# Performance work log

Measured on AMD Instinct MI355X. Metric: run time of the kernel, lower is better.

## Reference

```python
import jax, jax.numpy as jnp
import numpy as np

KS = 15       # erosion kernel size (ones kernel -> flat erosion = local min)
R = 60        # guided filter box-blur size
EPS = 1e-4


def _box_blur(x, r):
    # kornia box_blur: same-size mean filter, reflect padding; even kernel pads
    # (r-1)//2 before and r-1-(r-1)//2 after, per kornia _compute_padding.
    pb = (r - 1) // 2
    pa = r - 1 - pb
    xp = jnp.pad(x, ((0, 0), (0, 0), (pb, pa), (pb, pa)), mode='reflect')
    one = jnp.asarray(0.0, x.dtype)
    s = jax.lax.reduce_window(xp, one, jax.lax.add, (1, 1, r, 1), (1, 1, 1, 1), 'VALID')
    s = jax.lax.reduce_window(s, one, jax.lax.add, (1, 1, 1, r), (1, 1, 1, 1), 'VALID')
    return s / jnp.asarray(r * r, x.dtype)


def _erosion(x, k):
    # kornia flat erosion with ones kernel, geodesic border: local min over kxk
    p = k // 2
    init = jnp.asarray(jnp.inf, x.dtype)
    pad = [(0, 0), (0, 0), (p, p), (p, p)]
    e = jax.lax.reduce_window(x, init, jax.lax.min, (1, 1, k, 1), (1, 1, 1, 1), [(0, 0), (0, 0), (p, p), (0, 0)])
    e = jax.lax.reduce_window(e, init, jax.lax.min, (1, 1, 1, k), (1, 1, 1, 1), [(0, 0), (0, 0), (0, 0), (p, p)])
    return e


def setup_inputs() -> dict:
    key = jax.random.key(0)
    I = jax.random.uniform(key, (8, 3, 1080, 1920), dtype=jnp.float32)
    return {"I": I}


def reference(I) -> jnp.ndarray:
    # dark channel: per-pixel min over the 3 channels  [B,1,H,W]
    dark = jnp.min(I, axis=1, keepdims=True)
    # guided_filter_plus(dark)
    d_im = _erosion(dark, KS)
    mean_I = _box_blur(d_im, R)
    mean_p = _box_blur(dark, R)
    mean_Ip = _box_blur(d_im * dark, R)
    cov_Ip = mean_Ip - mean_I * mean_p
    mean_II = _box_blur(d_im * d_im, R)
    var_I = mean_II - mean_I * mean_I
    a = cov_Ip / (var_I + EPS)
    b = mean_p - a * mean_I
    mean_a = _box_blur(a, R)
    mean_b = _box_blur(b, R)
    q = mean_a * d_im + mean_b
    return q
```

## Files before the change

kernel.cpp:

```cpp
#include <hip/hip_runtime.h>
#include <hip/hip_fp16.h>

#define HH 1080
#define WW 1920
#define NB 8
#define HWP (HH*WW)
#define NPX (NB*HWP)
#define NCX (WW/2)

__device__ __forceinline__ int reflH(int y){ int r = y < 0 ? -y : y; return r >= HH ? 2*HH-2-r : r; }
__device__ __forceinline__ int reflW(int x){ int r = x < 0 ? -x : x; return r >= WW ? 2*WW-2-r : r; }

__global__ __launch_bounds__(256) void k_dark(const float* __restrict__ I, __half* __restrict__ dark){
    int q = blockIdx.x*blockDim.x + threadIdx.x;
    if (q >= NPX/4) return;
    int base = q*4;
    int b = base / HWP;
    int p = base - b*HWP;
    const float* src = I + (size_t)b*3*HWP + p;
    float4 c0 = *(const float4*)(src);
    float4 c1 = *(const float4*)(src + HWP);
    float4 c2 = *(const float4*)(src + 2*HWP);
    float m0 = fminf(fminf(c0.x, c1.x), c2.x);
    float m1 = fminf(fminf(c0.y, c1.y), c2.y);
    float m2 = fminf(fminf(c0.z, c1.z), c2.z);
    float m3 = fminf(fminf(c0.w, c1.w), c2.w);
    __half2* dst = (__half2*)(dark + base);
    dst[0] = __floats2half2_rn(m0, m1);
    dst[1] = __floats2half2_rn(m2, m3);
}

#define EV_T 60
__global__ __launch_bounds__(256) void k_erosv(const __half* __restrict__ in, __half* __restrict__ out){
    int t = blockIdx.x*blockDim.x + threadIdx.x;
    if (t >= NCX*NB*(HH/EV_T)) return;
    int cx = t % NCX;
    int r  = t / NCX;
    int b  = r % NB;
    int y0 = (r / NB) * EV_T;
    const __half2* src = (const __half2*)(in  + (size_t)b*HWP) + cx;
    __half2*       dst = (__half2*)(out + (size_t)b*HWP) + cx;
    float2 w[15];
    #pragma unroll
    for (int k = 0; k < 14; ++k){
        int y = y0 - 7 + k;
        if (y >= 0 && y < HH) w[k] = __half22float2(src[(size_t)y*NCX]);
        else { w[k].x = 1e5f; w[k].y = 1e5f; }
    }
    for (int y = y0; y < y0 + EV_T; ++y){
        int yn = y + 7;
        if (yn < HH) w[14] = __half22float2(src[(size_t)yn*NCX]);
        else { w[14].x = 1e5f; w[14].y = 1e5f; }
        float ax[8], ay[8];
        #pragma unroll
        for (int k = 0; k < 7; ++k){ ax[k] = fminf(w[2*k].x, w[2*k+1].x); ay[k] = fminf(w[2*k].y, w[2*k+1].y); }
        ax[7] = w[14].x; ay[7] = w[14].y;
        #pragma unroll
        for (int k = 0; k < 4; ++k){ ax[k] = fminf(ax[k], ax[k+4]); ay[k] = fminf(ay[k], ay[k+4]); }
        float mx = fminf(fminf(ax[0], ax[1]), fminf(ax[2], ax[3]));
        float my = fminf(fminf(ay[0], ay[1]), fminf(ay[2], ay[3]));
        dst[(size_t)y*NCX] = __floats2half2_rn(mx, my);
        #pragma unroll
        for (int k = 0; k < 14; ++k) w[k] = w[k+1];
    }
}

__global__ __launch_bounds__(256) void k_erosh(const __half* __restrict__ in, __half* __restrict__ out){
    __shared__ __half2 lds[264];
    int bid = blockIdx.x;
    int seg = bid & 3;
    int y   = (bid >> 2) % HH;
    int b   = bid / (4*HH);
    int seg0 = seg * 512;
    const __half* row = in + (size_t)b*HWP + (size_t)y*WW;
    int tid = threadIdx.x;
    for (int slot = tid; slot < 264; slot += 256){
        int x = seg0 - 8 + 2*slot;
        __half2 v;
        if (x >= 0 && x + 1 < WW) v = *(const __half2*)(row + x);
        else {
            float lo = (x   >= 0 && x   < WW) ? __half2float(row[x])   : 1e5f;
            float hi = (x+1 >= 0 && x+1 < WW) ? __half2float(row[x+1]) : 1e5f;
            v = __floats2half2_rn(lo, hi);
        }
        lds[slot] = v;
    }
    __syncthreads();
    int x0 = seg0 + 2*tid;
    if (x0 >= WW) return;
    float v[18];
    #pragma unroll
    for (int k = 0; k < 9; ++k){
        float2 f = __half22float2(lds[tid + k]);
        v[2*k] = f.x; v[2*k+1] = f.y;
    }
    float c = v[2];
    #pragma unroll
    for (int k = 3; k <= 15; ++k) c = fminf(c, v[k]);
    float o0 = fminf(c, v[1]);
    float o1 = fminf(c, v[16]);
    *(__half2*)(out + (size_t)b*HWP + (size_t)y*WW + x0) = __floats2half2_rn(o0, o1);
}

#define BV_T 54
__global__ __launch_bounds__(256) void k_blurv4(const __half* __restrict__ pdim, const __half* __restrict__ pdark,
                                                __half* __restrict__ v0, __half* __restrict__ v1,
                                                __half* __restrict__ v2, __half* __restrict__ v3){
    int t = blockIdx.x*blockDim.x + threadIdx.x;
    if (t >= NCX*NB*(HH/BV_T)) return;
    int cx = t % NCX;
    int r  = t / NCX;
    int b  = r % NB;
    int y0 = (r / NB) * BV_T;
    size_t pb = (size_t)b*HWP;
    const __half2* pd = (const __half2*)(pdim  + pb) + cx;
    const __half2* pk = (const __half2*)(pdark + pb) + cx;
    __half2* o0 = (__half2*)(v0 + pb) + cx;
    __half2* o1 = (__half2*)(v1 + pb) + cx;
    __half2* o2 = (__half2*)(v2 + pb) + cx;
    __half2* o3 = (__half2*)(v3 + pb) + cx;

    float si0=0,si1=0,sp0=0,sp1=0,sip0=0,sip1=0,sii0=0,sii1=0;
    auto acc = [&](int yy, float sg){
        int yr = reflH(yy);
        float2 di = __half22float2(pd[(size_t)yr*NCX]);
        float2 dk = __half22float2(pk[(size_t)yr*NCX]);
        si0  += sg*di.x;        si1  += sg*di.y;
        sp0  += sg*dk.x;        sp1  += sg*dk.y;
        sip0 += sg*(di.x*dk.x); sip1 += sg*(di.y*dk.y);
        sii0 += sg*(di.x*di.x); sii1 += sg*(di.y*di.y);
    };
    const float inv = 1.0f/60.0f;
    for (int k = -29; k <= 30; ++k) acc(y0 + k, 1.0f);
    size_t off = (size_t)y0*NCX;
    o0[off] = __floats2half2_rn(si0*inv,  si1*inv);
    o1[off] = __floats2half2_rn(sp0*inv,  sp1*inv);
    o2[off] = __floats2half2_rn(sip0*inv, sip1*inv);
    o3[off] = __floats2half2_rn(sii0*inv, sii1*inv);
    for (int y = y0 + 1; y < y0 + BV_T; ++y){
        acc(y + 30, 1.0f);
        acc(y - 30, -1.0f);
        off = (size_t)y*NCX;
        o0[off] = __floats2half2_rn(si0*inv,  si1*inv);
        o1[off] = __floats2half2_rn(sp0*inv,  sp1*inv);
        o2[off] = __floats2half2_rn(sip0*inv, sip1*inv);
        o3[off] = __floats2half2_rn(sii0*inv, sii1*inv);
    }
}

__global__ __launch_bounds__(256) void k_blurv2(const __half* __restrict__ pa, const __half* __restrict__ pbf,
                                                __half* __restrict__ va, __half* __restrict__ vb){
    int t = blockIdx.x*blockDim.x + threadIdx.x;
    if (t >= NCX*NB*(HH/BV_T)) return;
    int cx = t % NCX;
    int r  = t / NCX;
    int b  = r % NB;
    int y0 = (r / NB) * BV_T;
    size_t pbase = (size_t)b*HWP;
    const __half2* p0 = (const __half2*)(pa  + pbase) + cx;
    const __half2* p1 = (const __half2*)(pbf + pbase) + cx;
    __half2* o0 = (__half2*)(va + pbase) + cx;
    __half2* o1 = (__half2*)(vb + pbase) + cx;
    float sa0=0,sa1=0,sb0=0,sb1=0;
    auto acc = [&](int yy, float sg){
        int yr = reflH(yy);
        float2 fa = __half22float2(p0[(size_t)yr*NCX]);
        float2 fb = __half22float2(p1[(size_t)yr*NCX]);
        sa0 += sg*fa.x; sa1 += sg*fa.y;
        sb0 += sg*fb.x; sb1 += sg*fb.y;
    };
    const float inv = 1.0f/60.0f;
    for (int k = -29; k <= 30; ++k) acc(y0 + k, 1.0f);
    size_t off = (size_t)y0*NCX;
    o0[off] = __floats2half2_rn(sa0*inv, sa1*inv);
    o1[off] = __floats2half2_rn(sb0*inv, sb1*inv);
    for (int y = y0 + 1; y < y0 + BV_T; ++y){
        acc(y + 30, 1.0f);
        acc(y - 30, -1.0f);
        off = (size_t)y*NCX;
        o0[off] = __floats2half2_rn(sa0*inv, sa1*inv);
        o1[off] = __floats2half2_rn(sb0*inv, sb1*inv);
    }
}

#define PADI(e) ((e) + ((e) >> 5))

__global__ __launch_bounds__(128) void k_blurh4(const __half* __restrict__ v0, const __half* __restrict__ v1,
                                                const __half* __restrict__ v2, const __half* __restrict__ v3,
                                                __half* __restrict__ pa, __half* __restrict__ pbf){
    __shared__ float lds[4][2048];
    int bid = blockIdx.x;
    int y = bid % HH;
    int b = bid / HH;
    size_t rb = (size_t)b*HWP + (size_t)y*WW;
    const __half* p0 = v0 + rb; const __half* p1 = v1 + rb;
    const __half* p2 = v2 + rb; const __half* p3 = v3 + rb;
    int tid = threadIdx.x;
    for (int e = tid; e < 1979; e += 128){
        int x = reflW(e - 29);
        int pe = PADI(e);
        lds[0][pe] = __half2float(p0[x]);
        lds[1][pe] = __half2float(p1[x]);
        lds[2][pe] = __half2float(p2[x]);
        lds[3][pe] = __half2float(p3[x]);
    }
    __syncthreads();
    if (tid >= 120) return;
    int x0 = tid * 16;
    float s0=0, s1=0, s2=0, s3=0;
    for (int k = 0; k < 60; ++k){
        int pe = PADI(x0 + k);
        s0 += lds[0][pe]; s1 += lds[1][pe]; s2 += lds[2][pe]; s3 += lds[3][pe];
    }
    const float inv = 1.0f/60.0f;
    __half2 ha[8], hb[8];
    float prev_a = 0.f, prev_b = 0.f;
    #pragma unroll
    for (int j = 0; j < 16; ++j){
        if (j > 0){
            int pe1 = PADI(x0 + j + 59), pe0 = PADI(x0 + j - 1);
            s0 += lds[0][pe1] - lds[0][pe0];
            s1 += lds[1][pe1] - lds[1][pe0];
            s2 += lds[2][pe1] - lds[2][pe0];
            s3 += lds[3][pe1] - lds[3][pe0];
        }
        float mI  = s0*inv, mP = s1*inv, mIp = s2*inv, mII = s3*inv;
        float cov = mIp - mI*mP;
        float var = mII - mI*mI;
        float a   = cov / (var + 1e-4f);
        float bb  = mP - a*mI;
        if (j & 1){
            ha[j>>1] = __floats2half2_rn(prev_a, a);
            hb[j>>1] = __floats2half2_rn(prev_b, bb);
        } else { prev_a = a; prev_b = bb; }
    }
    *(uint4*)(pa  + rb + x0)     = *(uint4*)&ha[0];
    *(uint4*)(pa  + rb + x0 + 8) = *(uint4*)&ha[4];
    *(uint4*)(pbf + rb + x0)     = *(uint4*)&hb[0];
    *(uint4*)(pbf + rb + x0 + 8) = *(uint4*)&hb[4];
}

__global__ __launch_bounds__(128) void k_blurh2(const __half* __restrict__ va, const __half* __restrict__ vb,
                                                const __half* __restrict__ pdim, float* __restrict__ qout){
    __shared__ float lds[2][2048];
    int bid = blockIdx.x;
    int y = bid % HH;
    int b = bid / HH;
    size_t rb = (size_t)b*HWP + (size_t)y*WW;
    const __half* p0 = va + rb; const __half* p1 = vb + rb;
    int tid = threadIdx.x;
    for (int e = tid; e < 1979; e += 128){
        int x = reflW(e - 29);
        int pe = PADI(e);
        lds[0][pe] = __half2float(p0[x]);
        lds[1][pe] = __half2float(p1[x]);
    }
    __syncthreads();
    if (tid >= 120) return;
    int x0 = tid * 16;
    float sa=0, sb=0;
    for (int k = 0; k < 60; ++k){
        int pe = PADI(x0 + k);
        sa += lds[0][pe]; sb += lds[1][pe];
    }
    const float inv = 1.0f/60.0f;
    float qv[16];
    #pragma unroll
    for (int j = 0; j < 16; ++j){
        if (j > 0){
            int pe1 = PADI(x0 + j + 59), pe0 = PADI(x0 + j - 1);
            sa += lds[0][pe1] - lds[0][pe0];
            sb += lds[1][pe1] - lds[1][pe0];
        }
        float dv = __half2float(pdim[rb + x0 + j]);
        qv[j] = (sa*inv)*dv + (sb*inv);
    }
    #pragma unroll
    for (int m = 0; m < 4; ++m){
        *(float4*)(qout + rb + x0 + 4*m) = make_float4(qv[4*m], qv[4*m+1], qv[4*m+2], qv[4*m+3]);
    }
}

extern "C" void kernel_launch(void* const* d_in, const int* in_sizes, int n_in,
                              void* d_out, int out_size, void* d_ws, size_t ws_size,
                              hipStream_t stream){
    const float* I = (const float*)d_in[0];
    float* qout = (float*)d_out;
    __half* ws = (__half*)d_ws;

    __half* p_dark = ws;
    __half* p_tmp  = ws + (size_t)NPX;
    __half* p_dim  = ws + 2*(size_t)NPX;
    __half* p_v0   = ws + 3*(size_t)NPX;
    __half* p_v1   = ws + 4*(size_t)NPX;
    __half* p_v2   = ws + 5*(size_t)NPX;
    __half* p_v3   = ws + 6*(size_t)NPX;
    __half* p_a    = p_dark;
    __half* p_b    = p_tmp;
    __half* p_va   = p_v0;
    __half* p_vb   = p_v1;

    k_dark  <<<NPX/4/256, 256, 0, stream>>>(I, p_dark);
    k_erosv <<<(NCX*NB*(HH/EV_T))/256, 256, 0, stream>>>(p_dark, p_tmp);
    k_erosh <<<NB*HH*4, 256, 0, stream>>>(p_tmp, p_dim);
    k_blurv4<<<(NCX*NB*(HH/BV_T))/256, 256, 0, stream>>>(p_dim, p_dark, p_v0, p_v1, p_v2, p_v3);
    k_blurh4<<<NB*HH, 128, 0, stream>>>(p_v0, p_v1, p_v2, p_v3, p_a, p_b);
    k_blurv2<<<(NCX*NB*(HH/BV_T))/256, 256, 0, stream>>>(p_a, p_b, p_va, p_vb);
    k_blurh2<<<NB*HH, 128, 0, stream>>>(p_va, p_vb, p_dim, qout);
}
```

Baseline: 300.8 us.

## Restructure pipeline into five fused kernels with 8-wide vector columns

Fuses the dark-channel computation with horizontal erosion, does the vertical erosion with packed fp16 min using a prefix/suffix scheme, and processes 8 columns per thread in the vertical blur kernels. It also fuses the horizontal moment blur, the a/b computation and the horizontal blur of a/b into one row kernel, and folds the final vertical blur into the output write. Intermediate traffic and launch count drop. The vertical kernels now launch only 300 blocks, so parallelism and occupancy may suffer, and the erosion order changes from vertical-then-horizontal to horizontal-then-vertical.

```diff
diff --git a/kernel.cpp b/kernel.cpp
--- a/kernel.cpp
+++ b/kernel.cpp
@@ -5,279 +5,350 @@
 #define WW 1920
 #define NB 8
 #define HWP (HH*WW)
-#define NPX (NB*HWP)
-#define NCX (WW/2)
+#define NPXs ((size_t)NB*HWP)
+#define NC8 (WW/8)
+
+#define PADI(e) ((e) + ((e) >> 5))
 
 __device__ __forceinline__ int reflH(int y){ int r = y < 0 ? -y : y; return r >= HH ? 2*HH-2-r : r; }
 __device__ __forceinline__ int reflW(int x){ int r = x < 0 ? -x : x; return r >= WW ? 2*WW-2-r : r; }
 
-__global__ __launch_bounds__(256) void k_dark(const float* __restrict__ I, __half* __restrict__ dark){
-    int q = blockIdx.x*blockDim.x + threadIdx.x;
-    if (q >= NPX/4) return;
-    int base = q*4;
-    int b = base / HWP;
-    int p = base - b*HWP;
-    const float* src = I + (size_t)b*3*HWP + p;
-    float4 c0 = *(const float4*)(src);
-    float4 c1 = *(const float4*)(src + HWP);
-    float4 c2 = *(const float4*)(src + 2*HWP);
-    float m0 = fminf(fminf(c0.x, c1.x), c2.x);
-    float m1 = fminf(fminf(c0.y, c1.y), c2.y);
-    float m2 = fminf(fminf(c0.z, c1.z), c2.z);
-    float m3 = fminf(fminf(c0.w, c1.w), c2.w);
-    __half2* dst = (__half2*)(dark + base);
-    dst[0] = __floats2half2_rn(m0, m1);
-    dst[1] = __floats2half2_rn(m2, m3);
-}
-
-#define EV_T 60
-__global__ __launch_bounds__(256) void k_erosv(const __half* __restrict__ in, __half* __restrict__ out){
-    int t = blockIdx.x*blockDim.x + threadIdx.x;
-    if (t >= NCX*NB*(HH/EV_T)) return;
-    int cx = t % NCX;
-    int r  = t / NCX;
-    int b  = r % NB;
-    int y0 = (r / NB) * EV_T;
-    const __half2* src = (const __half2*)(in  + (size_t)b*HWP) + cx;
-    __half2*       dst = (__half2*)(out + (size_t)b*HWP) + cx;
-    float2 w[15];
-    #pragma unroll
-    for (int k = 0; k < 14; ++k){
-        int y = y0 - 7 + k;
-        if (y >= 0 && y < HH) w[k] = __half22float2(src[(size_t)y*NCX]);
-        else { w[k].x = 1e5f; w[k].y = 1e5f; }
-    }
-    for (int y = y0; y < y0 + EV_T; ++y){
-        int yn = y + 7;
-        if (yn < HH) w[14] = __half22float2(src[(size_t)yn*NCX]);
-        else { w[14].x = 1e5f; w[14].y = 1e5f; }
-        float ax[8], ay[8];
-        #pragma unroll
-        for (int k = 0; k < 7; ++k){ ax[k] = fminf(w[2*k].x, w[2*k+1].x); ay[k] = fminf(w[2*k].y, w[2*k+1].y); }
-        ax[7] = w[14].x; ay[7] = w[14].y;
-        #pragma unroll
-        for (int k = 0; k < 4; ++k){ ax[k] = fminf(ax[k], ax[k+4]); ay[k] = fminf(ay[k], ay[k+4]); }
-        float mx = fminf(fminf(ax[0], ax[1]), fminf(ax[2], ax[3]));
-        float my = fminf(fminf(ay[0], ay[1]), fminf(ay[2], ay[3]));
-        dst[(size_t)y*NCX] = __floats2half2_rn(mx, my);
-        #pragma unroll
-        for (int k = 0; k < 14; ++k) w[k] = w[k+1];
-    }
-}
-
-__global__ __launch_bounds__(256) void k_erosh(const __half* __restrict__ in, __half* __restrict__ out){
-    __shared__ __half2 lds[264];
+__device__ __forceinline__ unsigned pkmin(unsigned a, unsigned b){
+    unsigned r; asm("v_pk_min_f16 %0, %1, %2" : "=v"(r) : "v"(a), "v"(b)); return r;
+}
+#define INF2 0x7C007C00u
+
+__global__ __launch_bounds__(256) void k_dark_eh(const float* __restrict__ I,
+                                                 __half* __restrict__ dark, __half* __restrict__ eh){
+    __shared__ float ds[2048];
     int bid = blockIdx.x;
-    int seg = bid & 3;
-    int y   = (bid >> 2) % HH;
-    int b   = bid / (4*HH);
-    int seg0 = seg * 512;
-    const __half* row = in + (size_t)b*HWP + (size_t)y*WW;
+    int y = bid % HH;
+    int b = bid / HH;
+    const float* row0 = I + (size_t)b*3*HWP + (size_t)y*WW;
+    size_t rb = (size_t)b*HWP + (size_t)y*WW;
     int tid = threadIdx.x;
-    for (int slot = tid; slot < 264; slot += 256){
-        int x = seg0 - 8 + 2*slot;
-        __half2 v;
-        if (x >= 0 && x + 1 < WW) v = *(const __half2*)(row + x);
-        else {
-            float lo = (x   >= 0 && x   < WW) ? __half2float(row[x])   : 1e5f;
-            float hi = (x+1 >= 0 && x+1 < WW) ? __half2float(row[x+1]) : 1e5f;
-            v = __floats2half2_rn(lo, hi);
-        }
-        lds[slot] = v;
+    if (tid < 240){
+        int x0 = tid*8;
+        float4 c00 = *(const float4*)(row0 + x0);
+        float4 c01 = *(const float4*)(row0 + x0 + 4);
+        float4 c10 = *(const float4*)(row0 + HWP + x0);
+        float4 c11 = *(const float4*)(row0 + HWP + x0 + 4);
+        float4 c20 = *(const float4*)(row0 + 2*HWP + x0);
+        float4 c21 = *(const float4*)(row0 + 2*HWP + x0 + 4);
+        float m[8];
+        m[0]=fminf(fminf(c00.x,c10.x),c20.x); m[1]=fminf(fminf(c00.y,c10.y),c20.y);
+        m[2]=fminf(fminf(c00.z,c10.z),c20.z); m[3]=fminf(fminf(c00.w,c10.w),c20.w);
+        m[4]=fminf(fminf(c01.x,c11.x),c21.x); m[5]=fminf(fminf(c01.y,c11.y),c21.y);
+        m[6]=fminf(fminf(c01.z,c11.z),c21.z); m[7]=fminf(fminf(c01.w,c11.w),c21.w);
+        __half2 hd[4];
+        #pragma unroll
+        for (int l=0;l<4;++l) hd[l] = __floats2half2_rn(m[2*l], m[2*l+1]);
+        *(uint4*)(dark + rb + x0) = *(uint4*)hd;
+        #pragma unroll
+        for (int i=0;i<8;++i) ds[PADI(x0+7+i)] = m[i];
+    } else if (tid == 240){
+        for (int i=0;i<7;++i) ds[PADI(i)] = 1e30f;
+    } else if (tid == 241){
+        for (int i=0;i<7;++i) ds[PADI(1927+i)] = 1e30f;
     }
     __syncthreads();
-    int x0 = seg0 + 2*tid;
-    if (x0 >= WW) return;
-    float v[18];
-    #pragma unroll
-    for (int k = 0; k < 9; ++k){
-        float2 f = __half22float2(lds[tid + k]);
-        v[2*k] = f.x; v[2*k+1] = f.y;
-    }
-    float c = v[2];
-    #pragma unroll
-    for (int k = 3; k <= 15; ++k) c = fminf(c, v[k]);
-    float o0 = fminf(c, v[1]);
-    float o1 = fminf(c, v[16]);
-    *(__half2*)(out + (size_t)b*HWP + (size_t)y*WW + x0) = __floats2half2_rn(o0, o1);
-}
-
-#define BV_T 54
-__global__ __launch_bounds__(256) void k_blurv4(const __half* __restrict__ pdim, const __half* __restrict__ pdark,
-                                                __half* __restrict__ v0, __half* __restrict__ v1,
-                                                __half* __restrict__ v2, __half* __restrict__ v3){
-    int t = blockIdx.x*blockDim.x + threadIdx.x;
-    if (t >= NCX*NB*(HH/BV_T)) return;
-    int cx = t % NCX;
-    int r  = t / NCX;
-    int b  = r % NB;
-    int y0 = (r / NB) * BV_T;
-    size_t pb = (size_t)b*HWP;
-    const __half2* pd = (const __half2*)(pdim  + pb) + cx;
-    const __half2* pk = (const __half2*)(pdark + pb) + cx;
-    __half2* o0 = (__half2*)(v0 + pb) + cx;
-    __half2* o1 = (__half2*)(v1 + pb) + cx;
-    __half2* o2 = (__half2*)(v2 + pb) + cx;
-    __half2* o3 = (__half2*)(v3 + pb) + cx;
-
-    float si0=0,si1=0,sp0=0,sp1=0,sip0=0,sip1=0,sii0=0,sii1=0;
-    auto acc = [&](int yy, float sg){
+    if (tid >= 240) return;
+    int x0 = tid*8;
+    float s[22];
+    #pragma unroll
+    for (int i=0;i<22;++i) s[i] = ds[PADI(x0+i)];
+    float t1[21], t2[19], t4[15];
+    #pragma unroll
+    for (int i=0;i<21;++i) t1[i] = fminf(s[i], s[i+1]);
+    #pragma unroll
+    for (int i=0;i<19;++i) t2[i] = fminf(t1[i], t1[i+2]);
+    #pragma unroll
+    for (int i=0;i<15;++i) t4[i] = fminf(t2[i], t2[i+4]);
+    __half2 ho[4];
+    #pragma unroll
+    for (int l=0;l<4;++l){
+        float o0 = fminf(t4[2*l],   t4[2*l+7]);
+        float o1 = fminf(t4[2*l+1], t4[2*l+8]);
+        ho[l] = __floats2half2_rn(o0, o1);
+    }
+    *(uint4*)(eh + rb + x0) = *(uint4*)ho;
+}
+
+__global__ __launch_bounds__(256) void k_erosv(const __half* __restrict__ eh, __half* __restrict__ dim){
+    int t = blockIdx.x*256 + threadIdx.x;
+    int c8 = t % NC8;
+    int r  = t / NC8;
+    int b  = r & 7;
+    int y0 = (r >> 3) * 15;
+    const __half* sp = eh  + (size_t)b*HWP + (size_t)c8*8;
+    __half*       dp = dim + (size_t)b*HWP + (size_t)c8*8;
+    uint4 s[15];
+    #pragma unroll
+    for (int j=0;j<15;++j){
+        int y = y0 - 7 + j;
+        if ((unsigned)y < HH) s[j] = *(const uint4*)(sp + (size_t)y*WW);
+        else s[j] = make_uint4(INF2,INF2,INF2,INF2);
+    }
+    #pragma unroll
+    for (int j=13;j>=0;--j){
+        s[j].x = pkmin(s[j].x, s[j+1].x); s[j].y = pkmin(s[j].y, s[j+1].y);
+        s[j].z = pkmin(s[j].z, s[j+1].z); s[j].w = pkmin(s[j].w, s[j+1].w);
+    }
+    *(uint4*)(dp + (size_t)y0*WW) = s[0];
+    uint4 P = make_uint4(INF2,INF2,INF2,INF2);
+    #pragma unroll
+    for (int j=1;j<15;++j){
+        int y = y0 + 7 + j;
+        uint4 nv;
+        if ((unsigned)y < HH) nv = *(const uint4*)(sp + (size_t)y*WW);
+        else nv = make_uint4(INF2,INF2,INF2,INF2);
+        P.x = pkmin(P.x, nv.x); P.y = pkmin(P.y, nv.y);
+        P.z = pkmin(P.z, nv.z); P.w = pkmin(P.w, nv.w);
+        uint4 o;
+        o.x = pkmin(s[j].x, P.x); o.y = pkmin(s[j].y, P.y);
+        o.z = pkmin(s[j].z, P.z); o.w = pkmin(s[j].w, P.w);
+        *(uint4*)(dp + (size_t)(y0+j)*WW) = o;
+    }
+}
+
+#define BT 27
+__global__ __launch_bounds__(256) void k_blurv4(const __half* __restrict__ dimp, const __half* __restrict__ darkp,
+                                                __half* __restrict__ m0, __half* __restrict__ m1,
+                                                __half* __restrict__ m2, __half* __restrict__ m3){
+    int t = blockIdx.x*256 + threadIdx.x;
+    int c8 = t % NC8;
+    int r  = t / NC8;
+    int b  = r & 7;
+    int y0 = (r >> 3) * BT;
+    size_t base = (size_t)b*HWP + (size_t)c8*8;
+    const __half* pd = dimp + base;
+    const __half* pk = darkp + base;
+    float sI[8], sP[8], sIP[8], sII[8];
+    #pragma unroll
+    for (int i=0;i<8;++i){ sI[i]=0.f; sP[i]=0.f; sIP[i]=0.f; sII[i]=0.f; }
+    auto accA = [&](int yy){
         int yr = reflH(yy);
-        float2 di = __half22float2(pd[(size_t)yr*NCX]);
-        float2 dk = __half22float2(pk[(size_t)yr*NCX]);
-        si0  += sg*di.x;        si1  += sg*di.y;
-        sp0  += sg*dk.x;        sp1  += sg*dk.y;
-        sip0 += sg*(di.x*dk.x); sip1 += sg*(di.y*dk.y);
-        sii0 += sg*(di.x*di.x); sii1 += sg*(di.y*di.y);
+        uint4 vd = *(const uint4*)(pd + (size_t)yr*WW);
+        uint4 vk = *(const uint4*)(pk + (size_t)yr*WW);
+        const __half2* hd = (const __half2*)&vd;
+        const __half2* hk = (const __half2*)&vk;
+        #pragma unroll
+        for (int l=0;l<4;++l){
+            float2 fd = __half22float2(hd[l]);
+            float2 fk = __half22float2(hk[l]);
+            sI[2*l]+=fd.x; sI[2*l+1]+=fd.y;
+            sP[2*l]+=fk.x; sP[2*l+1]+=fk.y;
+            sIP[2*l]+=fd.x*fk.x; sIP[2*l+1]+=fd.y*fk.y;
+            sII[2*l]+=fd.x*fd.x; sII[2*l+1]+=fd.y*fd.y;
+        }
+    };
+    auto accS = [&](int yy){
+        int yr = reflH(yy);
+        uint4 vd = *(const uint4*)(pd + (size_t)yr*WW);
+        uint4 vk = *(const uint4*)(pk + (size_t)yr*WW);
+        const __half2* hd = (const __half2*)&vd;
+        const __half2* hk = (const __half2*)&vk;
+        #pragma unroll
+        for (int l=0;l<4;++l){
+            float2 fd = __half22float2(hd[l]);
+            float2 fk = __half22float2(hk[l]);
+            sI[2*l]-=fd.x; sI[2*l+1]-=fd.y;
+            sP[2*l]-=fk.x; sP[2*l+1]-=fk.y;
+            sIP[2*l]-=fd.x*fk.x; sIP[2*l+1]-=fd.y*fk.y;
+            sII[2*l]-=fd.x*fd.x; sII[2*l+1]-=fd.y*fd.y;
+        }
     };
     const float inv = 1.0f/60.0f;
-    for (int k = -29; k <= 30; ++k) acc(y0 + k, 1.0f);
-    size_t off = (size_t)y0*NCX;
-    o0[off] = __floats2half2_rn(si0*inv,  si1*inv);
-    o1[off] = __floats2half2_rn(sp0*inv,  sp1*inv);
-    o2[off] = __floats2half2_rn(sip0*inv, sip1*inv);
-    o3[off] = __floats2half2_rn(sii0*inv, sii1*inv);
-    for (int y = y0 + 1; y < y0 + BV_T; ++y){
-        acc(y + 30, 1.0f);
-        acc(y - 30, -1.0f);
-        off = (size_t)y*NCX;
-        o0[off] = __floats2half2_rn(si0*inv,  si1*inv);
-        o1[off] = __floats2half2_rn(sp0*inv,  sp1*inv);
-        o2[off] = __floats2half2_rn(sip0*inv, sip1*inv);
-        o3[off] = __floats2half2_rn(sii0*inv, sii1*inv);
-    }
-}
-
-__global__ __launch_bounds__(256) void k_blurv2(const __half* __restrict__ pa, const __half* __restrict__ pbf,
-                                                __half* __restrict__ va, __half* __restrict__ vb){
-    int t = blockIdx.x*blockDim.x + threadIdx.x;
-    if (t >= NCX*NB*(HH/BV_T)) return;
-    int cx = t % NCX;
-    int r  = t / NCX;
-    int b  = r % NB;
-    int y0 = (r / NB) * BV_T;
-    size_t pbase = (size_t)b*HWP;
-    const __half2* p0 = (const __half2*)(pa  + pbase) + cx;
-    const __half2* p1 = (const __half2*)(pbf + pbase) + cx;
-    __half2* o0 = (__half2*)(va + pbase) + cx;
-    __half2* o1 = (__half2*)(vb + pbase) + cx;
-    float sa0=0,sa1=0,sb0=0,sb1=0;
-    auto acc = [&](int yy, float sg){
-        int yr = reflH(yy);
-        float2 fa = __half22float2(p0[(size_t)yr*NCX]);
-        float2 fb = __half22float2(p1[(size_t)yr*NCX]);
-        sa0 += sg*fa.x; sa1 += sg*fa.y;
-        sb0 += sg*fb.x; sb1 += sg*fb.y;
-    };
-    const float inv = 1.0f/60.0f;
-    for (int k = -29; k <= 30; ++k) acc(y0 + k, 1.0f);
-    size_t off = (size_t)y0*NCX;
-    o0[off] = __floats2half2_rn(sa0*inv, sa1*inv);
-    o1[off] = __floats2half2_rn(sb0*inv, sb1*inv);
-    for (int y = y0 + 1; y < y0 + BV_T; ++y){
-        acc(y + 30, 1.0f);
-        acc(y - 30, -1.0f);
-        off = (size_t)y*NCX;
-        o0[off] = __floats2half2_rn(sa0*inv, sa1*inv);
-        o1[off] = __floats2half2_rn(sb0*inv, sb1*inv);
-    }
-}
-
-#define PADI(e) ((e) + ((e) >> 5))
-
-__global__ __launch_bounds__(128) void k_blurh4(const __half* __restrict__ v0, const __half* __restrict__ v1,
-                                                const __half* __restrict__ v2, const __half* __restrict__ v3,
-                                                __half* __restrict__ pa, __half* __restrict__ pbf){
-    __shared__ float lds[4][2048];
+    for (int k=-29;k<=30;++k) accA(y0+k);
+    auto emit = [&](int y){
+        size_t off = base + (size_t)y*WW;
+        __half2 h[4];
+        #pragma unroll
+        for (int l=0;l<4;++l) h[l] = __floats2half2_rn(sI[2*l]*inv, sI[2*l+1]*inv);
+        *(uint4*)(m0 + off) = *(uint4*)h;
+        #pragma unroll
+        for (int l=0;l<4;++l) h[l] = __floats2half2_rn(sP[2*l]*inv, sP[2*l+1]*inv);
+        *(uint4*)(m1 + off) = *(uint4*)h;
+        #pragma unroll
+        for (int l=0;l<4;++l) h[l] = __floats2half2_rn(sIP[2*l]*inv, sIP[2*l+1]*inv);
+        *(uint4*)(m2 + off) = *(uint4*)h;
+        #pragma unroll
+        for (int l=0;l<4;++l) h[l] = __floats2half2_rn(sII[2*l]*inv, sII[2*l+1]*inv);
+        *(uint4*)(m3 + off) = *(uint4*)h;
+    };
+    emit(y0);
+    for (int y=y0+1; y<y0+BT; ++y){
+        accA(y+30);
+        accS(y-30);
+        emit(y);
+    }
+}
+
+__global__ __launch_bounds__(256) void k_hab(const __half* __restrict__ m0, const __half* __restrict__ m1,
+                                             const __half* __restrict__ m2, const __half* __restrict__ m3,
+                                             __half* __restrict__ aH, __half* __restrict__ bH){
+    __shared__ float mom[4][2104];
+    __shared__ float ab[2][2040];
     int bid = blockIdx.x;
     int y = bid % HH;
     int b = bid / HH;
     size_t rb = (size_t)b*HWP + (size_t)y*WW;
-    const __half* p0 = v0 + rb; const __half* p1 = v1 + rb;
-    const __half* p2 = v2 + rb; const __half* p3 = v3 + rb;
     int tid = threadIdx.x;
-    for (int e = tid; e < 1979; e += 128){
-        int x = reflW(e - 29);
-        int pe = PADI(e);
-        lds[0][pe] = __half2float(p0[x]);
-        lds[1][pe] = __half2float(p1[x]);
-        lds[2][pe] = __half2float(p2[x]);
-        lds[3][pe] = __half2float(p3[x]);
+    if (tid < 240){
+        int x0 = tid*8;
+        int e0 = x0 + 58;
+        const __half* mp0 = m0 + rb; const __half* mp1 = m1 + rb;
+        const __half* mp2 = m2 + rb; const __half* mp3 = m3 + rb;
+        uint4 v; const __half2* h = (const __half2*)&v;
+        v = *(const uint4*)(mp0 + x0);
+        #pragma unroll
+        for (int l=0;l<4;++l){ float2 f=__half22float2(h[l]); mom[0][PADI(e0+2*l)]=f.x; mom[0][PADI(e0+2*l+1)]=f.y; }
+        v = *(const uint4*)(mp1 + x0);
+        #pragma unroll
+        for (int l=0;l<4;++l){ float2 f=__half22float2(h[l]); mom[1][PADI(e0+2*l)]=f.x; mom[1][PADI(e0+2*l+1)]=f.y; }
+        v = *(const uint4*)(mp2 + x0);
+        #pragma unroll
+        for (int l=0;l<4;++l){ float2 f=__half22float2(h[l]); mom[2][PADI(e0+2*l)]=f.x; mom[2][PADI(e0+2*l+1)]=f.y; }
+        v = *(const uint4*)(mp3 + x0);
+        #pragma unroll
+        for (int l=0;l<4;++l){ float2 f=__half22float2(h[l]); mom[3][PADI(e0+2*l)]=f.x; mom[3][PADI(e0+2*l+1)]=f.y; }
+    } else {
+        int h0 = (tid-240)*8;
+        for (int i=0;i<8;++i){
+            int hh = h0 + i;
+            if (hh >= 118) break;
+            int e = hh < 58 ? hh : 1978 + (hh-58);
+            int x = reflW(e - 58);
+            int pe = PADI(e);
+            mom[0][pe] = __half2float(m0[rb+x]);
+            mom[1][pe] = __half2float(m1[rb+x]);
+            mom[2][pe] = __half2float(m2[rb+x]);
+            mom[3][pe] = __half2float(m3[rb+x]);
+        }
     }
     __syncthreads();
-    if (tid >= 120) return;
-    int x0 = tid * 16;
-    float s0=0, s1=0, s2=0, s3=0;
-    for (int k = 0; k < 60; ++k){
-        int pe = PADI(x0 + k);
-        s0 += lds[0][pe]; s1 += lds[1][pe]; s2 += lds[2][pe]; s3 += lds[3][pe];
+    if (tid < 62){
+        int p0 = tid*32;
+        int cnt = min(32, 1979 - p0);
+        float S0=0,S1=0,S2=0,S3=0;
+        for (int k=0;k<60;++k){
+            int pe = PADI(p0+k);
+            S0 += mom[0][pe]; S1 += mom[1][pe]; S2 += mom[2][pe]; S3 += mom[3][pe];
+        }
+        const float inv = 1.0f/60.0f;
+        for (int j=0;j<cnt;++j){
+            if (j){
+                int iA = PADI(p0+j+59), iS = PADI(p0+j-1);
+                S0 += mom[0][iA]-mom[0][iS]; S1 += mom[1][iA]-mom[1][iS];
+                S2 += mom[2][iA]-mom[2][iS]; S3 += mom[3][iA]-mom[3][iS];
+            }
+            float mI=S0*inv, mP=S1*inv, mIp=S2*inv, mII=S3*inv;
+            float cov = mIp - mI*mP;
+            float var = mII - mI*mI;
+            float a = cov / (var + 1e-4f);
+            int pp = PADI(p0+j);
+            ab[0][pp] = a;
+            ab[1][pp] = mP - a*mI;
+        }
+    }
+    __syncthreads();
+    if (tid >= 60) return;
+    int x0 = tid*32;
+    float sa=0.f, sb=0.f;
+    for (int k=0;k<60;++k){
+        int pe = PADI(x0+k);
+        sa += ab[0][pe]; sb += ab[1][pe];
     }
     const float inv = 1.0f/60.0f;
-    __half2 ha[8], hb[8];
-    float prev_a = 0.f, prev_b = 0.f;
-    #pragma unroll
-    for (int j = 0; j < 16; ++j){
-        if (j > 0){
-            int pe1 = PADI(x0 + j + 59), pe0 = PADI(x0 + j - 1);
-            s0 += lds[0][pe1] - lds[0][pe0];
-            s1 += lds[1][pe1] - lds[1][pe0];
-            s2 += lds[2][pe1] - lds[2][pe0];
-            s3 += lds[3][pe1] - lds[3][pe0];
-        }
-        float mI  = s0*inv, mP = s1*inv, mIp = s2*inv, mII = s3*inv;
-        float cov = mIp - mI*mP;
-        float var = mII - mI*mI;
-        float a   = cov / (var + 1e-4f);
-        float bb  = mP - a*mI;
+    __half2 ha[16], hb[16];
+    float pa_=0.f, pb_=0.f;
+    #pragma unroll
+    for (int j=0;j<32;++j){
+        if (j){
+            int iA = PADI(x0+j+59), iS = PADI(x0+j-1);
+            sa += ab[0][iA]-ab[0][iS];
+            sb += ab[1][iA]-ab[1][iS];
+        }
+        float av = sa*inv, bv = sb*inv;
         if (j & 1){
-            ha[j>>1] = __floats2half2_rn(prev_a, a);
-            hb[j>>1] = __floats2half2_rn(prev_b, bb);
-        } else { prev_a = a; prev_b = bb; }
-    }
-    *(uint4*)(pa  + rb + x0)     = *(uint4*)&ha[0];
-    *(uint4*)(pa  + rb + x0 + 8) = *(uint4*)&ha[4];
-    *(uint4*)(pbf + rb + x0)     = *(uint4*)&hb[0];
-    *(uint4*)(pbf + rb + x0 + 8) = *(uint4*)&hb[4];
-}
-
-__global__ __launch_bounds__(128) void k_blurh2(const __half* __restrict__ va, const __half* __restrict__ vb,
-                                                const __half* __restrict__ pdim, float* __restrict__ qout){
-    __shared__ float lds[2][2048];
-    int bid = blockIdx.x;
-    int y = bid % HH;
-    int b = bid / HH;
-    size_t rb = (size_t)b*HWP + (size_t)y*WW;
-    const __half* p0 = va + rb; const __half* p1 = vb + rb;
-    int tid = threadIdx.x;
-    for (int e = tid; e < 1979; e += 128){
-        int x = reflW(e - 29);
-        int pe = PADI(e);
-        lds[0][pe] = __half2float(p0[x]);
-        lds[1][pe] = __half2float(p1[x]);
-    }
-    __syncthreads();
-    if (tid >= 120) return;
-    int x0 = tid * 16;
-    float sa=0, sb=0;
-    for (int k = 0; k < 60; ++k){
-        int pe = PADI(x0 + k);
-        sa += lds[0][pe]; sb += lds[1][pe];
-    }
+            ha[j>>1] = __floats2half2_rn(pa_, av);
+            hb[j>>1] = __floats2half2_rn(pb_, bv);
+        } else { pa_ = av; pb_ = bv; }
+    }
+    *(uint4*)(aH+rb+x0)    = *(uint4*)&ha[0];
+    *(uint4*)(aH+rb+x0+8)  = *(uint4*)&ha[4];
+    *(uint4*)(aH+rb+x0+16) = *(uint4*)&ha[8];
+    *(uint4*)(aH+rb+x0+24) = *(uint4*)&ha[12];
+    *(uint4*)(bH+rb+x0)    = *(uint4*)&hb[0];
+    *(uint4*)(bH+rb+x0+8)  = *(uint4*)&hb[4];
+    *(uint4*)(bH+rb+x0+16) = *(uint4*)&hb[8];
+    *(uint4*)(bH+rb+x0+24) = *(uint4*)&hb[12];
+}
+
+__global__ __launch_bounds__(256) void k_final(const __half* __restrict__ aHp, const __half* __restrict__ bHp,
+                                               const __half* __restrict__ dimp, float* __restrict__ q){
+    int t = blockIdx.x*256 + threadIdx.x;
+    int c8 = t % NC8;
+    int r  = t / NC8;
+    int b  = r & 7;
+    int y0 = (r >> 3) * BT;
+    size_t base = (size_t)b*HWP + (size_t)c8*8;
+    const __half* pa = aHp + base;
+    const __half* pb = bHp + base;
+    const __half* pd = dimp + base;
+    float* pq = q + base;
+    float sa[8], sb[8];
+    #pragma unroll
+    for (int i=0;i<8;++i){ sa[i]=0.f; sb[i]=0.f; }
+    auto accA = [&](int yy){
+        int yr = reflH(yy);
+        uint4 va = *(const uint4*)(pa + (size_t)yr*WW);
+        uint4 vb = *(const uint4*)(pb + (size_t)yr*WW);
+        const __half2* hA = (const __half2*)&va;
+        const __half2* hB = (const __half2*)&vb;
+        #pragma unroll
+        for (int l=0;l<4;++l){
+            float2 fa = __half22float2(hA[l]);
+            float2 fb = __half22float2(hB[l]);
+            sa[2*l]+=fa.x; sa[2*l+1]+=fa.y;
+            sb[2*l]+=fb.x; sb[2*l+1]+=fb.y;
+        }
+    };
+    auto accS = [&](int yy){
+        int yr = reflH(yy);
+        uint4 va = *(const uint4*)(pa + (size_t)yr*WW);
+        uint4 vb = *(const uint4*)(pb + (size_t)yr*WW);
+        const __half2* hA = (const __half2*)&va;
+        const __half2* hB = (const __half2*)&vb;
+        #pragma unroll
+        for (int l=0;l<4;++l){
+            float2 fa = __half22float2(hA[l]);
+            float2 fb = __half22float2(hB[l]);
+            sa[2*l]-=fa.x; sa[2*l+1]-=fa.y;
+            sb[2*l]-=fb.x; sb[2*l+1]-=fb.y;
+        }
+    };
     const float inv = 1.0f/60.0f;
-    float qv[16];
-    #pragma unroll
-    for (int j = 0; j < 16; ++j){
-        if (j > 0){
-            int pe1 = PADI(x0 + j + 59), pe0 = PADI(x0 + j - 1);
-            sa += lds[0][pe1] - lds[0][pe0];
-            sb += lds[1][pe1] - lds[1][pe0];
-        }
-        float dv = __half2float(pdim[rb + x0 + j]);
-        qv[j] = (sa*inv)*dv + (sb*inv);
-    }
-    #pragma unroll
-    for (int m = 0; m < 4; ++m){
-        *(float4*)(qout + rb + x0 + 4*m) = make_float4(qv[4*m], qv[4*m+1], qv[4*m+2], qv[4*m+3]);
+    for (int k=-29;k<=30;++k) accA(y0+k);
+    auto emit = [&](int y){
+        uint4 vd = *(const uint4*)(pd + (size_t)y*WW);
+        const __half2* hd = (const __half2*)&vd;
+        float qv[8];
+        #pragma unroll
+        for (int l=0;l<4;++l){
+            float2 fd = __half22float2(hd[l]);
+            qv[2*l]   = (sa[2*l]*inv)*fd.x + sb[2*l]*inv;
+            qv[2*l+1] = (sa[2*l+1]*inv)*fd.y + sb[2*l+1]*inv;
+        }
+        float* o = pq + (size_t)y*WW;
+        *(float4*)o     = make_float4(qv[0],qv[1],qv[2],qv[3]);
+        *(float4*)(o+4) = make_float4(qv[4],qv[5],qv[6],qv[7]);
+    };
+    emit(y0);
+    for (int y=y0+1; y<y0+BT; ++y){
+        accA(y+30);
+        accS(y-30);
+        emit(y);
     }
 }
 
@@ -289,22 +360,18 @@
     __half* ws = (__half*)d_ws;
 
     __half* p_dark = ws;
-    __half* p_tmp  = ws + (size_t)NPX;
-    __half* p_dim  = ws + 2*(size_t)NPX;
-    __half* p_v0   = ws + 3*(size_t)NPX;
-    __half* p_v1   = ws + 4*(size_t)NPX;
-    __half* p_v2   = ws + 5*(size_t)NPX;
-    __half* p_v3   = ws + 6*(size_t)NPX;
-    __half* p_a    = p_dark;
-    __half* p_b    = p_tmp;
-    __half* p_va   = p_v0;
-    __half* p_vb   = p_v1;
-
-    k_dark  <<<NPX/4/256, 256, 0, stream>>>(I, p_dark);
-    k_erosv <<<(NCX*NB*(HH/EV_T))/256, 256, 0, stream>>>(p_dark, p_tmp);
-    k_erosh <<<NB*HH*4, 256, 0, stream>>>(p_tmp, p_dim);
-    k_blurv4<<<(NCX*NB*(HH/BV_T))/256, 256, 0, stream>>>(p_dim, p_dark, p_v0, p_v1, p_v2, p_v3);
-    k_blurh4<<<NB*HH, 128, 0, stream>>>(p_v0, p_v1, p_v2, p_v3, p_a, p_b);
-    k_blurv2<<<(NCX*NB*(HH/BV_T))/256, 256, 0, stream>>>(p_a, p_b, p_va, p_vb);
-    k_blurh2<<<NB*HH, 128, 0, stream>>>(p_va, p_vb, p_dim, qout);
-}
+    __half* p_eh   = ws + NPXs;
+    __half* p_dim  = ws + 2*NPXs;
+    __half* p_m0   = ws + 3*NPXs;
+    __half* p_m1   = ws + 4*NPXs;
+    __half* p_m2   = ws + 5*NPXs;
+    __half* p_m3   = ws + 6*NPXs;
+    __half* p_aH   = p_dark;
+    __half* p_bH   = p_eh;
+
+    k_dark_eh<<<NB*HH, 256, 0, stream>>>(I, p_dark, p_eh);
+    k_erosv  <<<540,   256, 0, stream>>>(p_eh, p_dim);
+    k_blurv4 <<<300,   256, 0, stream>>>(p_dim, p_dark, p_m0, p_m1, p_m2, p_m3);
+    k_hab    <<<NB*HH, 256, 0, stream>>>(p_m0, p_m1, p_m2, p_m3, p_aH, p_bH);
+    k_final  <<<300,   256, 0, stream>>>(p_aH, p_bH, p_dim, qout);
+}
```

Result: slower. 316.6 us (+5.2%).
